# Kernel optimization log

Hardware: AMD Instinct MI355X
Metric: run time of the kernel (lower is better)

## Reference

```python
import jax, jax.numpy as jnp
import numpy as np

BATCH, SEQ, EMBED, HIDDEN, VOCAB = 32, 64, 512, 512, 32000

def setup_inputs() -> dict:
    key = jax.random.key(0)
    ks = jax.random.split(key, 11)
    s = lambda k, shape, scale: jax.random.normal(k, shape, dtype=jnp.float32) * scale
    return {
        "features": s(ks[0], (BATCH, HIDDEN), 1.0),
        "captions": jax.random.randint(ks[1], (BATCH, SEQ), 0, VOCAB),
        "embedding": s(ks[2], (VOCAB, EMBED), 1.0),
        "Wz_w": s(ks[3], (HIDDEN, EMBED + HIDDEN), 0.03),
        "Wz_b": s(ks[4], (HIDDEN,), 0.03),
        "Wr_w": s(ks[5], (HIDDEN, EMBED + HIDDEN), 0.03),
        "Wr_b": s(ks[6], (HIDDEN,), 0.03),
        "Wh_w": s(ks[7], (HIDDEN, EMBED + HIDDEN), 0.03),
        "Wh_b": s(ks[8], (HIDDEN,), 0.03),
        "fc_w": s(ks[9], (VOCAB, HIDDEN), 0.03),
        "fc_b": s(ks[10], (VOCAB,), 0.03),
    }

def reference(features, captions, embedding, Wz_w, Wz_b, Wr_w, Wr_b, Wh_w, Wh_b, fc_w, fc_b):
    # embeddings: [B, T, E] -> scan over time with xs [T, B, E]
    emb = embedding[captions]                      # [B, T, E]
    xs = jnp.swapaxes(emb, 0, 1)                   # [T, B, E]

    def step(h, x_t):
        comb = jnp.concatenate([x_t, h], axis=1)                   # [B, E+H]
        z = jax.nn.sigmoid(comb @ Wz_w.T + Wz_b)                   # update gate
        r = jax.nn.sigmoid(comb @ Wr_w.T + Wr_b)                   # reset gate
        comb_r = jnp.concatenate([x_t, r * h], axis=1)
        h_tilde = jnp.tanh(comb_r @ Wh_w.T + Wh_b)
        h_new = (1.0 - z) * h + z * h_tilde
        return h_new, h_new

    _, hs = jax.lax.scan(step, features, xs)       # hs: [T, B, H]
    hs = jnp.swapaxes(hs, 0, 1)                    # [B, T, H]
    # output projection done once over all timesteps (same math as per-step fc_out)
    logits = jnp.einsum('bth,vh->btv', hs, fc_w) + fc_b  # [B, T, V]
    return logits
```

## Files before the change

kernel.cpp:

```cpp
#include <hip/hip_runtime.h>
#include <hip/hip_bf16.h>

typedef __bf16 bf16;
typedef __bf16 bf16x8 __attribute__((ext_vector_type(8)));
typedef float f32x4 __attribute__((ext_vector_type(4)));
typedef unsigned int u32x4 __attribute__((ext_vector_type(4)));

#define B_SZ 32
#define T_SZ 64
#define H_SZ 512
#define V_SZ 32000
#define NWG_REC 8
#define NTILES 250
#define MTILES 16

__device__ __forceinline__ float sigmoidf_(float v) { return 1.0f / (1.0f + expf(-v)); }

__device__ __forceinline__ bf16x8 cvt8(const float* __restrict__ p) {
  float4 a = *(const float4*)p;
  float4 b = *(const float4*)(p + 4);
  bf16x8 o;
  o[0] = (bf16)a.x; o[1] = (bf16)a.y; o[2] = (bf16)a.z; o[3] = (bf16)a.w;
  o[4] = (bf16)b.x; o[5] = (bf16)b.y; o[6] = (bf16)b.z; o[7] = (bf16)b.w;
  return o;
}

#define GLD(dst, base, off) \
  asm volatile("global_load_dwordx4 %0, %1, off offset:" off " sc0 sc1" \
               : "=v"(dst) : "v"(base))
#define GST2(base, off, val) do { \
  unsigned int w_ = (unsigned int)__builtin_bit_cast(unsigned short, (bf16)(val)); \
  asm volatile("global_store_short %0, %1, off offset:" off " sc0 sc1" \
               :: "v"(base), "v"(w_) : "memory"); \
} while (0)
#define WAITV  asm volatile("s_waitcnt vmcnt(0)" ::: "memory")
#define SCHEDB __builtin_amdgcn_sched_barrier(0)

__device__ __forceinline__ int llc_poll(const int* p) {
  int r;
  asm volatile("global_load_dword %0, %1, off sc0 sc1\n\ts_waitcnt vmcnt(0)"
               : "=v"(r) : "v"(p) : "memory");
  return r;
}

__global__ void prep_k(const float* __restrict__ feat, bf16* __restrict__ h_g,
                       int* __restrict__ ctr,
                       const float* __restrict__ Wz, const float* __restrict__ Wr,
                       const float* __restrict__ Wh, bf16* __restrict__ dst) {
  int i = blockIdx.x * blockDim.x + threadIdx.x;
  int w = i >> 15;
  int rem = i & 32767;
  int n = rem >> 6;
  int k8 = (rem & 63) * 8;
  const float* W = (w == 0) ? Wz : (w == 1) ? Wr : Wh;
  *(bf16x8*)(dst + (long)w * 262144 + n * 512 + k8) = cvt8(W + (long)n * 1024 + 512 + k8);
  if (i < B_SZ * H_SZ) h_g[i] = (bf16)feat[i];
  if (i < 128) ctr[i] = 0;
}

__global__ __launch_bounds__(256) void xproj_k(
    const int* __restrict__ caps, const float* __restrict__ emb,
    const float* __restrict__ B0, const float* __restrict__ B1, const float* __restrict__ B2,
    const float* __restrict__ bias0, const float* __restrict__ bias1, const float* __restrict__ bias2,
    float* __restrict__ C, int gemm_blocks,
    const float* __restrict__ fcw_src, bf16* __restrict__ fcw_dst)
{
  __shared__ __align__(16) bf16 lA[128 * 32];
  __shared__ __align__(16) bf16 lB[128 * 32];
  const int tid = threadIdx.x;

  if ((int)blockIdx.x >= gemm_blocks) {
    long base = ((long)(blockIdx.x - gemm_blocks) * 256 + tid) * 8;
    const long stride = (long)128 * 256 * 8;
    for (long i = base; i < (long)V_SZ * H_SZ; i += stride)
      *(bf16x8*)(fcw_dst + i) = cvt8(fcw_src + i);
    return;
  }

  const int lane = tid & 63;
  const int l15  = lane & 15;
  const int kb8  = (lane >> 4) * 8;
  const int wid  = tid >> 6;
  const int wm   = wid >> 1, wn = wid & 1;
  const int wg   = blockIdx.x;
  const int mtile = wg % 16, ntile = wg / 16;
  const int m0 = mtile * 128, n0 = ntile * 128;

  int wsel = n0 >> 9;
  const float* Bv   = wsel == 0 ? B0 : wsel == 1 ? B1 : B2;
  const float* bias = wsel == 0 ? bias0 : wsel == 1 ? bias1 : bias2;
  int nb = n0 & 511;

  f32x4 acc[4][4] = {};

  for (int k0 = 0; k0 < 512; k0 += 32) {
    #pragma unroll
    for (int j = 0; j < 2; ++j) {
      int c = j * 256 + tid;
      int row = c >> 2;
      int kc = (c & 3) * 8;
      *(bf16x8*)&lA[row * 32 + kc] = cvt8(emb + (long)caps[m0 + row] * 512 + k0 + kc);
      *(bf16x8*)&lB[row * 32 + kc] = cvt8(Bv + (long)(nb + row) * 1024 + k0 + kc);
    }
    __syncthreads();
    bf16x8 af[4], bfr[4];
    #pragma unroll
    for (int mf = 0; mf < 4; ++mf)
      af[mf] = *(const bf16x8*)&lA[(wm * 64 + mf * 16 + l15) * 32 + kb8];
    #pragma unroll
    for (int nf = 0; nf < 4; ++nf)
      bfr[nf] = *(const bf16x8*)&lB[(wn * 64 + nf * 16 + l15) * 32 + kb8];
    #pragma unroll
    for (int mf = 0; mf < 4; ++mf)
      #pragma unroll
      for (int nf = 0; nf < 4; ++nf)
        acc[mf][nf] = __builtin_amdgcn_mfma_f32_16x16x32_bf16(af[mf], bfr[nf], acc[mf][nf], 0, 0, 0);
    __syncthreads();
  }

  #pragma unroll
  for (int mf = 0; mf < 4; ++mf)
    #pragma unroll
    for (int nf = 0; nf < 4; ++nf)
      #pragma unroll
      for (int r = 0; r < 4; ++r) {
        int row = m0 + wm * 64 + mf * 16 + (lane >> 4) * 4 + r;
        int lc  = wn * 64 + nf * 16 + l15;
        C[(long)row * 1536 + n0 + lc] = acc[mf][nf][r] + bias[nb + lc];
      }
}

__global__ __launch_bounds__(512, 2) void fused_k(
    const float* __restrict__ X,
    const bf16* __restrict__ Wzh, const bf16* __restrict__ Wrh, const bf16* __restrict__ Whh,
    const float* __restrict__ feat,
    bf16* __restrict__ h_g, bf16* __restrict__ rh_g,
    bf16* __restrict__ hs, int* __restrict__ ctr,
    const bf16* __restrict__ fcw16, const float* __restrict__ fcw_f32,
    const float* __restrict__ fc_b, float* __restrict__ out, int use_bf16B)
{
  __shared__ __align__(16) char smem[20480];
  const int tid  = threadIdx.x;
  const int bid  = blockIdx.x;
  const int lane = tid & 63;
  const int l15  = lane & 15;
  int* prog = ctr + 64;

  if (bid < NWG_REC) {
    char* ldsb = smem;
    const int u    = bid * 8 + (tid >> 6);
    const int kb   = (lane >> 4) * 8;
    const int rq   = (lane >> 4) * 4;
    const int b0   = (u >> 5) * 16;
    const int gcol = (u & 31) * 16 + l15;

    u32x4 Bz[16], Br[16], Bh[16];
    #pragma unroll
    for (int kk = 0; kk < 16; ++kk) {
      Bz[kk] = *(const u32x4*)(Wzh + (long)gcol * 512 + kk * 32 + kb);
      Br[kk] = *(const u32x4*)(Wrh + (long)gcol * 512 + kk * 32 + kb);
      Bh[kk] = *(const u32x4*)(Whh + (long)gcol * 512 + kk * 32 + kb);
    }
    #pragma unroll
    for (int kk = 0; kk < 16; ++kk)
      asm volatile("" : "+v"(Bz[kk]), "+v"(Br[kk]), "+v"(Bh[kk]));

    float hprev[4];
    #pragma unroll
    for (int r = 0; r < 4; ++r) hprev[r] = feat[(b0 + rq + r) * 512 + gcol];

    const float* xb = X + (long)(b0 + rq) * 64 * 1536 + gcol;
    float xz[4], xr[4];
    #pragma unroll
    for (int r = 0; r < 4; ++r) {
      xz[r] = xb[r * 98304];
      xr[r] = xb[r * 98304 + 512];
    }

    const int srow0 = tid >> 6;
    const int soff0 = (tid * 16) ^ ((srow0 & 7) << 4);
    const int soff1 = (8192 + tid * 16) ^ ((srow0 & 7) << 4);
    const int fbase = (l15 * 1024 + (lane >> 4) * 16) ^ ((l15 & 7) << 4);

    bf16* rhst = rh_g + (b0 + rq) * 512 + gcol;
    bf16* hst  = h_g  + (b0 + rq) * 512 + gcol;

    int epoch = 0;
    for (int t = 0; t < T_SZ; ++t) {
      {
        const bf16* src = h_g + b0 * 512;
        u32x4 v0, v1;
        GLD(v0, src + tid * 8, "0");
        GLD(v1, src + 4096 + tid * 8, "0");
        WAITV;
        SCHEDB;
        *(u32x4*)(ldsb + soff0) = v0;
        *(u32x4*)(ldsb + soff1) = v1;
      }
      __syncthreads();
      f32x4 ze = {}, re = {};
      #pragma unroll
      for (int kk = 0; kk < 16; ++kk) {
        bf16x8 a = *(const bf16x8*)(ldsb + (fbase ^ (kk * 64)));
        ze = __builtin_amdgcn_mfma_f32_16x16x32_bf16(a, __builtin_bit_cast(bf16x8, Bz[kk]), ze, 0, 0, 0);
        re = __builtin_amdgcn_mfma_f32_16x16x32_bf16(a, __builtin_bit_cast(bf16x8, Br[kk]), re, 0, 0, 0);
      }
      float xh[4];
      #pragma unroll
      for (int r = 0; r < 4; ++r) xh[r] = xb[r * 98304 + t * 1536 + 1024];
      f32x4 zf;
      {
        float r0 = sigmoidf_(re[0] + xr[0]) * hprev[0];
        float r1 = sigmoidf_(re[1] + xr[1]) * hprev[1];
        float r2 = sigmoidf_(re[2] + xr[2]) * hprev[2];
        float r3 = sigmoidf_(re[3] + xr[3]) * hprev[3];
        GST2(rhst, "0", r0); GST2(rhst, "1024", r1); GST2(rhst, "2048", r2); GST2(rhst, "3072", r3);
        #pragma unroll
        for (int r = 0; r < 4; ++r) zf[r] = sigmoidf_(ze[r] + xz[r]);
      }
      ++epoch;
      asm volatile("s_waitcnt vmcnt(0) lgkmcnt(0)" ::: "memory");
      __syncthreads();
      if (tid == 0) {
        __hip_atomic_fetch_add(ctr, 1, __ATOMIC_RELAXED, __HIP_MEMORY_SCOPE_AGENT);
        while (__hip_atomic_load(ctr, __ATOMIC_RELAXED, __HIP_MEMORY_SCOPE_AGENT) < NWG_REC * epoch)
          __builtin_amdgcn_s_sleep(1);
      }
      __syncthreads();

      {
        const bf16* src = rh_g + b0 * 512;
        u32x4 v0, v1;
        GLD(v0, src + tid * 8, "0");
        GLD(v1, src + 4096 + tid * 8, "0");
        WAITV;
        SCHEDB;
        *(u32x4*)(ldsb + soff0) = v0;
        *(u32x4*)(ldsb + soff1) = v1;
      }
      __syncthreads();
      f32x4 he = {};
      #pragma unroll
      for (int kk = 0; kk < 16; ++kk) {
        bf16x8 a = *(const bf16x8*)(ldsb + (fbase ^ (kk * 64)));
        he = __builtin_amdgcn_mfma_f32_16x16x32_bf16(a, __builtin_bit_cast(bf16x8, Bh[kk]), he, 0, 0, 0);
      }
      if (t + 1 < T_SZ) {
        #pragma unroll
        for (int r = 0; r < 4; ++r) {
          xz[r] = xb[r * 98304 + (t + 1) * 1536];
          xr[r] = xb[r * 98304 + (t + 1) * 1536 + 512];
        }
      }
      bf16* ph = hs + (long)(t * 32 + b0 + rq) * 512 + gcol;
      #pragma unroll
      for (int r = 0; r < 4; ++r) {
        float ht = tanhf(he[r] + xh[r]);
        float hn = hprev[r] + zf[r] * (ht - hprev[r]);
        hprev[r] = hn;
      }
      GST2(hst, "0", hprev[0]); GST2(hst, "1024", hprev[1]);
      GST2(hst, "2048", hprev[2]); GST2(hst, "3072", hprev[3]);
      GST2(ph, "0", hprev[0]); GST2(ph, "1024", hprev[1]);
      GST2(ph, "2048", hprev[2]); GST2(ph, "3072", hprev[3]);
      ++epoch;
      asm volatile("s_waitcnt vmcnt(0) lgkmcnt(0)" ::: "memory");
      __syncthreads();
      if (tid == 0) {
        __hip_atomic_fetch_add(ctr, 1, __ATOMIC_RELAXED, __HIP_MEMORY_SCOPE_AGENT);
        while (__hip_atomic_load(ctr, __ATOMIC_RELAXED, __HIP_MEMORY_SCOPE_AGENT) < NWG_REC * epoch)
          __builtin_amdgcn_s_sleep(1);
        if (bid == 0) {
          int e = epoch;
          asm volatile("global_store_dword %0, %1, off sc0 sc1" :: "v"(prog), "v"(e) : "memory");
        }
      }
      __syncthreads();
    }
    return;
  }

  const int lwg   = bid - NWG_REC;
  const int mtile = lwg / NTILES;
  const int ntile = lwg % NTILES;
  const int m0 = mtile * 128, n0 = ntile * 128;

  if (tid == 0) {
    const int tgt = 8 * (mtile + 1);
    while (llc_poll(prog) < tgt) __builtin_amdgcn_s_sleep(32);
  }
  __syncthreads();

  bf16* lA = (bf16*)smem;
  bf16* lB = (bf16*)(smem + 10240);
  const int kb8  = (lane >> 4) * 8;
  const int wid  = tid >> 6;
  const int wm   = wid >> 1;
  const int wn   = wid & 1;
  const int arow = tid >> 2;
  const int akc  = (tid & 3) * 8;

  f32x4 acc[2][4] = {};

  for (int k0 = 0; k0 < 512; k0 += 32) {
    u32x4 av;
    GLD(av, hs + (long)(m0 + arow) * 512 + k0 + akc, "0");
    bf16x8 bv;
    if (use_bf16B) bv = *(const bf16x8*)(fcw16 + (long)(n0 + arow) * 512 + k0 + akc);
    else           bv = cvt8(fcw_f32 + (long)(n0 + arow) * 512 + k0 + akc);
    WAITV;
    SCHEDB;
    *(u32x4*)&lA[arow * 40 + akc] = av;
    *(bf16x8*)&lB[arow * 40 + akc] = bv;
    __syncthreads();
    bf16x8 af[2], bfr[4];
    #pragma unroll
    for (int mf = 0; mf < 2; ++mf)
      af[mf] = *(const bf16x8*)&lA[(wm * 32 + mf * 16 + l15) * 40 + kb8];
    #pragma unroll
    for (int nf = 0; nf < 4; ++nf)
      bfr[nf] = *(const bf16x8*)&lB[(wn * 64 + nf * 16 + l15) * 40 + kb8];
    #pragma unroll
    for (int mf = 0; mf < 2; ++mf)
      #pragma unroll
      for (int nf = 0; nf < 4; ++nf)
        acc[mf][nf] = __builtin_amdgcn_mfma_f32_16x16x32_bf16(af[mf], bfr[nf], acc[mf][nf], 0, 0, 0);
    __syncthreads();
  }

  #pragma unroll
  for (int mf = 0; mf < 2; ++mf)
    #pragma unroll
    for (int nf = 0; nf < 4; ++nf) {
      int col = n0 + wn * 64 + nf * 16 + l15;
      float bias_v = fc_b[col];
      #pragma unroll
      for (int r = 0; r < 4; ++r) {
        int rr = m0 + wm * 32 + mf * 16 + (lane >> 4) * 4 + r;
        int tt = rr >> 5, b = rr & 31;
        out[(long)(b * 64 + tt) * 32000 + col] = acc[mf][nf][r] + bias_v;
      }
    }
}

extern "C" void kernel_launch(void* const* d_in, const int* in_sizes, int n_in,
                              void* d_out, int out_size, void* d_ws, size_t ws_size,
                              hipStream_t stream) {
  const float* feat = (const float*)d_in[0];
  const int*   caps = (const int*)d_in[1];
  const float* emb  = (const float*)d_in[2];
  const float* Wz_w = (const float*)d_in[3];
  const float* Wz_b = (const float*)d_in[4];
  const float* Wr_w = (const float*)d_in[5];
  const float* Wr_b = (const float*)d_in[6];
  const float* Wh_w = (const float*)d_in[7];
  const float* Wh_b = (const float*)d_in[8];
  const float* fc_w = (const float*)d_in[9];
  const float* fc_b = (const float*)d_in[10];
  float* out = (float*)d_out;

  char* ws = (char*)d_ws;
  float* X_all = (float*)(ws + 0);
  bf16*  h_g   = (bf16*) (ws + 12582912);
  bf16*  rh_g  = (bf16*) (ws + 12615680);
  bf16*  hs    = (bf16*) (ws + 12648448);
  bf16*  Whp   = (bf16*) (ws + 14745600);
  int*   ctr   = (int*)  (ws + 16318464);
  bf16*  fcw16 = (bf16*) (ws + 16318976);
  const bool cvt_fc = (ws_size >= (size_t)49087000);

  prep_k<<<dim3(384), dim3(256), 0, stream>>>(feat, h_g, ctr, Wz_w, Wr_w, Wh_w, Whp);

  xproj_k<<<dim3(cvt_fc ? 320 : 192), dim3(256), 0, stream>>>(
      caps, emb, Wz_w, Wr_w, Wh_w, Wz_b, Wr_b, Wh_b, X_all, 192, fc_w, fcw16);

  fused_k<<<dim3(NWG_REC + MTILES * NTILES), dim3(512), 0, stream>>>(
      X_all, Whp, Whp + 262144, Whp + 524288, feat, h_g, rh_g, hs, ctr,
      fcw16, fc_w, fc_b, out, cvt_fc ? 1 : 0);
}
```

Baseline: 650.9 us.

## Fold prep into xproj launch, stream Wh from memory, relax occupancy bound

Merges the prep kernel (weight conversion, h init, counter reset) into the xproj kernel as extra blocks, which removes one launch. The recurrent workgroups now keep only the Wz and Wr fragments in registers, loaded via explicit asm loads, and re-read Wh from global/L2 each step instead of holding it. The launch bound drops from 2 to 1 block per CU, and the wait before each barrier no longer waits on lgkmcnt. This frees registers in the latency-critical recurrence, but it adds per-step global loads of Wh on the serial path and lowers occupancy for the projection tiles that share the kernel.

Measured after the change: 646.8 us. Within noise of the previous version (-0.6%).

```diff
diff --git a/kernel.cpp b/kernel.cpp
--- a/kernel.cpp
+++ b/kernel.cpp
@@ -28,6 +28,12 @@
 #define GLD(dst, base, off) \
   asm volatile("global_load_dwordx4 %0, %1, off offset:" off " sc0 sc1" \
                : "=v"(dst) : "v"(base))
+#define LOADALL(af, base) do { \
+  GLD(af[0],  base, "0");   GLD(af[1],  base, "64");  GLD(af[2],  base, "128"); GLD(af[3],  base, "192"); \
+  GLD(af[4],  base, "256"); GLD(af[5],  base, "320"); GLD(af[6],  base, "384"); GLD(af[7],  base, "448"); \
+  GLD(af[8],  base, "512"); GLD(af[9],  base, "576"); GLD(af[10], base, "640"); GLD(af[11], base, "704"); \
+  GLD(af[12], base, "768"); GLD(af[13], base, "832"); GLD(af[14], base, "896"); GLD(af[15], base, "960"); \
+} while (0)
 #define GST2(base, off, val) do { \
   unsigned int w_ = (unsigned int)__builtin_bit_cast(unsigned short, (bf16)(val)); \
   asm volatile("global_store_short %0, %1, off offset:" off " sc0 sc1" \
@@ -43,34 +49,35 @@
   return r;
 }
 
-__global__ void prep_k(const float* __restrict__ feat, bf16* __restrict__ h_g,
-                       int* __restrict__ ctr,
-                       const float* __restrict__ Wz, const float* __restrict__ Wr,
-                       const float* __restrict__ Wh, bf16* __restrict__ dst) {
-  int i = blockIdx.x * blockDim.x + threadIdx.x;
-  int w = i >> 15;
-  int rem = i & 32767;
-  int n = rem >> 6;
-  int k8 = (rem & 63) * 8;
-  const float* W = (w == 0) ? Wz : (w == 1) ? Wr : Wh;
-  *(bf16x8*)(dst + (long)w * 262144 + n * 512 + k8) = cvt8(W + (long)n * 1024 + 512 + k8);
-  if (i < B_SZ * H_SZ) h_g[i] = (bf16)feat[i];
-  if (i < 128) ctr[i] = 0;
-}
-
 __global__ __launch_bounds__(256) void xproj_k(
     const int* __restrict__ caps, const float* __restrict__ emb,
     const float* __restrict__ B0, const float* __restrict__ B1, const float* __restrict__ B2,
     const float* __restrict__ bias0, const float* __restrict__ bias1, const float* __restrict__ bias2,
-    float* __restrict__ C, int gemm_blocks,
-    const float* __restrict__ fcw_src, bf16* __restrict__ fcw_dst)
+    float* __restrict__ C, int gemm_blocks, int prep_start,
+    const float* __restrict__ fcw_src, bf16* __restrict__ fcw_dst,
+    const float* __restrict__ feat, bf16* __restrict__ h_g, int* __restrict__ ctr,
+    bf16* __restrict__ whp_dst)
 {
   __shared__ __align__(16) bf16 lA[128 * 32];
   __shared__ __align__(16) bf16 lB[128 * 32];
   const int tid = threadIdx.x;
-
-  if ((int)blockIdx.x >= gemm_blocks) {
-    long base = ((long)(blockIdx.x - gemm_blocks) * 256 + tid) * 8;
+  const int bidx = blockIdx.x;
+
+  if (bidx >= prep_start) {
+    int i = (bidx - prep_start) * 256 + tid;
+    int w = i >> 15;
+    int rem = i & 32767;
+    int n = rem >> 6;
+    int k8 = (rem & 63) * 8;
+    const float* W = (w == 0) ? B0 : (w == 1) ? B1 : B2;
+    *(bf16x8*)(whp_dst + (long)w * 262144 + n * 512 + k8) = cvt8(W + (long)n * 1024 + 512 + k8);
+    if (i < B_SZ * H_SZ) h_g[i] = (bf16)feat[i];
+    if (i < 128) ctr[i] = 0;
+    return;
+  }
+
+  if (bidx >= gemm_blocks) {
+    long base = ((long)(bidx - gemm_blocks) * 256 + tid) * 8;
     const long stride = (long)128 * 256 * 8;
     for (long i = base; i < (long)V_SZ * H_SZ; i += stride)
       *(bf16x8*)(fcw_dst + i) = cvt8(fcw_src + i);
@@ -82,8 +89,7 @@
   const int kb8  = (lane >> 4) * 8;
   const int wid  = tid >> 6;
   const int wm   = wid >> 1, wn = wid & 1;
-  const int wg   = blockIdx.x;
-  const int mtile = wg % 16, ntile = wg / 16;
+  const int mtile = bidx % 16, ntile = bidx / 16;
   const int m0 = mtile * 128, n0 = ntile * 128;
 
   int wsel = n0 >> 9;
@@ -130,7 +136,7 @@
       }
 }
 
-__global__ __launch_bounds__(512, 2) void fused_k(
+__global__ __launch_bounds__(512, 1) void fused_k(
     const float* __restrict__ X,
     const bf16* __restrict__ Wzh, const bf16* __restrict__ Wrh, const bf16* __restrict__ Whh,
     const float* __restrict__ feat,
@@ -154,16 +160,11 @@
     const int b0   = (u >> 5) * 16;
     const int gcol = (u & 31) * 16 + l15;
 
-    u32x4 Bz[16], Br[16], Bh[16];
-    #pragma unroll
-    for (int kk = 0; kk < 16; ++kk) {
-      Bz[kk] = *(const u32x4*)(Wzh + (long)gcol * 512 + kk * 32 + kb);
-      Br[kk] = *(const u32x4*)(Wrh + (long)gcol * 512 + kk * 32 + kb);
-      Bh[kk] = *(const u32x4*)(Whh + (long)gcol * 512 + kk * 32 + kb);
-    }
-    #pragma unroll
-    for (int kk = 0; kk < 16; ++kk)
-      asm volatile("" : "+v"(Bz[kk]), "+v"(Br[kk]), "+v"(Bh[kk]));
+    u32x4 Bz[16], Br[16];
+    LOADALL(Bz, Wzh + (long)gcol * 512 + kb);
+    LOADALL(Br, Wrh + (long)gcol * 512 + kb);
+    WAITV;
+    const bf16* whb = Whh + (long)gcol * 512 + kb;
 
     float hprev[4];
     #pragma unroll
@@ -219,7 +220,7 @@
         for (int r = 0; r < 4; ++r) zf[r] = sigmoidf_(ze[r] + xz[r]);
       }
       ++epoch;
-      asm volatile("s_waitcnt vmcnt(0) lgkmcnt(0)" ::: "memory");
+      WAITV;
       __syncthreads();
       if (tid == 0) {
         __hip_atomic_fetch_add(ctr, 1, __ATOMIC_RELAXED, __HIP_MEMORY_SCOPE_AGENT);
@@ -243,7 +244,8 @@
       #pragma unroll
       for (int kk = 0; kk < 16; ++kk) {
         bf16x8 a = *(const bf16x8*)(ldsb + (fbase ^ (kk * 64)));
-        he = __builtin_amdgcn_mfma_f32_16x16x32_bf16(a, __builtin_bit_cast(bf16x8, Bh[kk]), he, 0, 0, 0);
+        u32x4 bh = *(const u32x4*)(whb + kk * 32);
+        he = __builtin_amdgcn_mfma_f32_16x16x32_bf16(a, __builtin_bit_cast(bf16x8, bh), he, 0, 0, 0);
       }
       if (t + 1 < T_SZ) {
         #pragma unroll
@@ -264,7 +266,7 @@
       GST2(ph, "0", hprev[0]); GST2(ph, "1024", hprev[1]);
       GST2(ph, "2048", hprev[2]); GST2(ph, "3072", hprev[3]);
       ++epoch;
-      asm volatile("s_waitcnt vmcnt(0) lgkmcnt(0)" ::: "memory");
+      WAITV;
       __syncthreads();
       if (tid == 0) {
         __hip_atomic_fetch_add(ctr, 1, __ATOMIC_RELAXED, __HIP_MEMORY_SCOPE_AGENT);
@@ -369,10 +371,10 @@
   bf16*  fcw16 = (bf16*) (ws + 16318976);
   const bool cvt_fc = (ws_size >= (size_t)49087000);
 
-  prep_k<<<dim3(384), dim3(256), 0, stream>>>(feat, h_g, ctr, Wz_w, Wr_w, Wh_w, Whp);
-
-  xproj_k<<<dim3(cvt_fc ? 320 : 192), dim3(256), 0, stream>>>(
-      caps, emb, Wz_w, Wr_w, Wh_w, Wz_b, Wr_b, Wh_b, X_all, 192, fc_w, fcw16);
+  const int prep_start = cvt_fc ? 320 : 192;
+  xproj_k<<<dim3(prep_start + 384), dim3(256), 0, stream>>>(
+      caps, emb, Wz_w, Wr_w, Wh_w, Wz_b, Wr_b, Wh_b, X_all, 192, prep_start,
+      fc_w, fcw16, feat, h_g, ctr, Whp);
 
   fused_k<<<dim3(NWG_REC + MTILES * NTILES), dim3(512), 0, stream>>>(
       X_all, Whp, Whp + 262144, Whp + 524288, feat, h_g, rh_g, hs, ctr,
```
